# Optimization experiments

Measured on AMD Instinct MI355X. Metric: run time of the kernel, lower is better.

Reference implementation:

```python
import jax, jax.numpy as jnp
import numpy as np

N_CHROM = 23
BINS_PER_CHROM = 5000
B = 16
S = 512  # sampled bins per (class, batch-row): 256 nonzeros + 256 sampled zeros
EOS_DIM = 512
BIN_DIM = 256
D_MODEL = 512
NUM_STATES = 3
VOCAB = N_CHROM * BINS_PER_CHROM


def setup_inputs() -> dict:
    key = jax.random.key(0)
    ks = jax.random.split(key, 9)
    return {
        "eos_emb": jax.random.normal(ks[0], (B, N_CHROM, EOS_DIM), dtype=jnp.float32),
        "sampled_indices": jax.random.randint(ks[1], (N_CHROM, B, S), 0, BINS_PER_CHROM),
        "targets": jax.random.randint(ks[2], (N_CHROM, B, S), 0, 3),
        "bin_embedding_table": jax.random.normal(ks[3], (VOCAB, BIN_DIM), dtype=jnp.float32) * 0.02,
        "W_bin": jax.random.normal(ks[4], (D_MODEL, BIN_DIM), dtype=jnp.float32) / np.sqrt(BIN_DIM),
        "W_eos": jax.random.normal(ks[5], (D_MODEL, EOS_DIM), dtype=jnp.float32) / np.sqrt(EOS_DIM),
        "b_eos": jax.random.normal(ks[6], (D_MODEL,), dtype=jnp.float32) * 0.01,
        "W_fc": jax.random.normal(ks[7], (NUM_STATES, 2 * D_MODEL), dtype=jnp.float32) / np.sqrt(2 * D_MODEL),
        "b_fc": jax.random.normal(ks[8], (NUM_STATES,), dtype=jnp.float32) * 0.01,
    }


def reference(eos_emb, sampled_indices, targets, bin_embedding_table, W_bin, W_eos, b_eos, W_fc, b_fc):
    # eos_projection (use_eos_proj=True): [B, C, eos_dim] -> [B, C, d_model]
    eos = jnp.einsum("bce,de->bcd", eos_emb, W_eos) + b_eos
    # vocab index per class: token_to_ind offset c*BINS_PER_CHROM + bin position
    offsets = (jnp.arange(N_CHROM, dtype=sampled_indices.dtype) * BINS_PER_CHROM)[:, None, None]
    ind = sampled_indices + offsets                      # [C, B, S]
    bin_emb = bin_embedding_table[ind]                   # [C, B, S, bin_dim]
    # bin_projection fires because bin_emb_dim != d_model (no bias)
    bin_proj = jnp.einsum("cbse,de->cbsd", bin_emb, W_bin)  # [C, B, S, d_model]
    # repeat eos_emb[:, c, :] across each row's sampled bins
    eos_rep = jnp.broadcast_to(jnp.transpose(eos, (1, 0, 2))[:, :, None, :], bin_proj.shape)
    total = jnp.concatenate([bin_proj, eos_rep], axis=-1)   # [C, B, S, 2*d_model]
    # fc: Linear(2*d_model, num_states) + ReLU
    pred = jax.nn.relu(jnp.einsum("cbsd,nd->cbsn", total, W_fc) + b_fc)
    return pred, targets
```

## Files before the change

kernel.cpp:

```cpp
#include <hip/hip_runtime.h>

#define N_CHROM 23
#define BINS_PER_CHROM 5000
#define BSZ 16
#define SSZ 512
#define EOS_DIM 512
#define BIN_DIM 256
#define D_MODEL 512
#define VOCAB (N_CHROM * BINS_PER_CHROM)
#define ROWS (N_CHROM * BSZ * SSZ)
#define PRED_SIZE (ROWS * 3)

#define WS_M    0
#define WS_MEOS 768
#define WS_PT   3456

__global__ __launch_bounds__(256) void precompute_M(
    const float* __restrict__ W_bin, const float* __restrict__ W_eos,
    const float* __restrict__ W_fc, float* __restrict__ M,
    float* __restrict__ Meos)
{
    __shared__ float wfc_s[3][512];
    __shared__ float red[3][8][32];
    const int bid = blockIdx.x;
    const bool isM = (bid < 8);
    const float* src = isM ? W_bin : W_eos;
    const int ld   = isM ? 256 : 512;
    const int wofs = isM ? 0 : 512;
    const int eb   = (isM ? bid : (bid - 8)) * 32;
    float* dst = isM ? M : Meos;

    const int t = threadIdx.x;
    for (int i = t; i < 3 * 512; i += 256) {
        int n = i >> 9, d = i & 511;
        wfc_s[n][d] = W_fc[n * 1024 + wofs + d];
    }
    __syncthreads();

    const int el = t & 31, slice = t >> 5;
    const int e = eb + el;
    float a0 = 0.f, a1 = 0.f, a2 = 0.f;
    const int d0 = slice * 64;
    for (int dd = 0; dd < 64; ++dd) {
        int d = d0 + dd;
        float v = src[d * ld + e];
        a0 += wfc_s[0][d] * v;
        a1 += wfc_s[1][d] * v;
        a2 += wfc_s[2][d] * v;
    }
    red[0][slice][el] = a0;
    red[1][slice][el] = a1;
    red[2][slice][el] = a2;
    __syncthreads();

    if (slice < 3) {
        float s = 0.f;
        for (int q = 0; q < 8; ++q) s += red[slice][q][el];
        dst[slice * ld + e] = s;
    }
}

__global__ __launch_bounds__(256) void project_table(
    const float* __restrict__ table, const float* __restrict__ M,
    float4* __restrict__ pt)
{
    const int wave = threadIdx.x >> 6, lane = threadIdx.x & 63;
    const int rbase = (blockIdx.x * 4 + wave) * 8;
    if (rbase >= VOCAB) return;

    const float4 m0 = ((const float4*)M)[lane];
    const float4 m1 = ((const float4*)M)[64 + lane];
    const float4 m2 = ((const float4*)M)[128 + lane];

    const float4* tb = (const float4*)table;
    float4 v[8];
#pragma unroll
    for (int k = 0; k < 8; ++k)
        v[k] = tb[(long long)(rbase + k) * 64 + lane];

#pragma unroll
    for (int k = 0; k < 8; ++k) {
        float p0 = v[k].x * m0.x + v[k].y * m0.y + v[k].z * m0.z + v[k].w * m0.w;
        float p1 = v[k].x * m1.x + v[k].y * m1.y + v[k].z * m1.z + v[k].w * m1.w;
        float p2 = v[k].x * m2.x + v[k].y * m2.y + v[k].z * m2.z + v[k].w * m2.w;
        for (int m = 32; m; m >>= 1) {
            p0 += __shfl_xor(p0, m);
            p1 += __shfl_xor(p1, m);
            p2 += __shfl_xor(p2, m);
        }
        if (lane == 0) pt[rbase + k] = make_float4(p0, p1, p2, 0.f);
    }
}

__global__ __launch_bounds__(256) void gather_out(
    const int* __restrict__ sampled, const int* __restrict__ targets,
    const float4* __restrict__ pt, const float* __restrict__ Meos,
    const float* __restrict__ eos_emb, const float* __restrict__ b_eos,
    const float* __restrict__ W_fc, const float* __restrict__ b_fc,
    float* __restrict__ out)
{
    __shared__ float ebc_s[3];
    const int r = blockIdx.x * 256 + threadIdx.x;
    const int cb = blockIdx.x >> 1;
    const int c = cb / BSZ, b = cb % BSZ;

    const int bin = sampled[r];
    const int tgt = targets[r];

    const int w = threadIdx.x >> 6, lane = threadIdx.x & 63;
    if (w < 3) {
        const float* eos = eos_emb + ((long long)b * N_CHROM + c) * EOS_DIM;
        const float* me  = Meos + w * 512;
        const float* wf2 = W_fc + w * 1024 + 512;
        float s = 0.f;
#pragma unroll
        for (int e0 = 0; e0 < 512; e0 += 64) {
            int e = e0 + lane;
            s += eos[e] * me[e] + wf2[e] * b_eos[e];
        }
        for (int m = 32; m; m >>= 1) s += __shfl_xor(s, m);
        if (lane == 0) ebc_s[w] = s + b_fc[w];
    }
    __syncthreads();

    const float4 p = pt[c * BINS_PER_CHROM + bin];
    const long long o = (long long)r * 3;
    out[o + 0] = fmaxf(p.x + ebc_s[0], 0.f);
    out[o + 1] = fmaxf(p.y + ebc_s[1], 0.f);
    out[o + 2] = fmaxf(p.z + ebc_s[2], 0.f);
    out[PRED_SIZE + r] = (float)tgt;
}

extern "C" void kernel_launch(void* const* d_in, const int* in_sizes, int n_in,
                              void* d_out, int out_size, void* d_ws, size_t ws_size,
                              hipStream_t stream) {
    const float* eos_emb = (const float*)d_in[0];
    const int*   sampled = (const int*)d_in[1];
    const int*   targets = (const int*)d_in[2];
    const float* table   = (const float*)d_in[3];
    const float* W_bin   = (const float*)d_in[4];
    const float* W_eos   = (const float*)d_in[5];
    const float* b_eos   = (const float*)d_in[6];
    const float* W_fc    = (const float*)d_in[7];
    const float* b_fc    = (const float*)d_in[8];
    float* out = (float*)d_out;
    float* ws  = (float*)d_ws;

    float*  M    = ws + WS_M;
    float*  Meos = ws + WS_MEOS;
    float4* pt   = (float4*)(ws + WS_PT);

    precompute_M<<<24, 256, 0, stream>>>(W_bin, W_eos, W_fc, M, Meos);
    project_table<<<(VOCAB / 8 + 3) / 4, 256, 0, stream>>>(table, M, pt);
    gather_out<<<ROWS / 256, 256, 0, stream>>>(sampled, targets, pt, Meos,
                                               eos_emb, b_eos, W_fc, b_fc, out);
}
```

Baseline: 203.5 us.

## Precompute per-(chrom,batch) eos bias once and use nontemporal loads/stores

Moves the eos-projection dot product out of the gather kernel, where it was recomputed by every 256-row block with a block sync. It now runs once per (chromosome, batch) pair in extra blocks prepended to the table-projection kernel, and the constant bias term is computed once in the weight precompute kernel. The table stream and the gather's index reads and output writes now use nontemporal loads and stores. The gather kernel becomes a simple load-add-store with no shared memory or barrier. This adds a few hundred small blocks to the projection launch.

```diff
diff --git a/kernel.cpp b/kernel.cpp
--- a/kernel.cpp
+++ b/kernel.cpp
@@ -10,15 +10,20 @@
 #define VOCAB (N_CHROM * BINS_PER_CHROM)
 #define ROWS (N_CHROM * BSZ * SSZ)
 #define PRED_SIZE (ROWS * 3)
+#define NCB (N_CHROM * BSZ)
 
-#define WS_M    0
-#define WS_MEOS 768
-#define WS_PT   3456
+#define WS_M     0
+#define WS_MEOS  768
+#define WS_CONST 2304
+#define WS_E     2432
+#define WS_PT    4096
+
+typedef float fvec4 __attribute__((ext_vector_type(4)));
 
 __global__ __launch_bounds__(256) void precompute_M(
     const float* __restrict__ W_bin, const float* __restrict__ W_eos,
-    const float* __restrict__ W_fc, float* __restrict__ M,
-    float* __restrict__ Meos)
+    const float* __restrict__ W_fc, const float* __restrict__ b_eos,
+    const float* __restrict__ b_fc, float* __restrict__ ws)
 {
     __shared__ float wfc_s[3][512];
     __shared__ float red[3][8][32];
@@ -28,7 +33,7 @@
     const int ld   = isM ? 256 : 512;
     const int wofs = isM ? 0 : 512;
     const int eb   = (isM ? bid : (bid - 8)) * 32;
-    float* dst = isM ? M : Meos;
+    float* dst = ws + (isM ? WS_M : WS_MEOS);
 
     const int t = threadIdx.x;
     for (int i = t; i < 3 * 512; i += 256) {
@@ -58,25 +63,58 @@
         for (int q = 0; q < 8; ++q) s += red[slice][q][el];
         dst[slice * ld + e] = s;
     }
+
+    if (bid == 0) {
+        const int wv = t >> 6, ln = t & 63;
+        if (wv < 3) {
+            const float* wf2 = W_fc + wv * 1024 + 512;
+            float s = 0.f;
+#pragma unroll
+            for (int e0 = 0; e0 < 512; e0 += 64) s += wf2[e0 + ln] * b_eos[e0 + ln];
+            for (int m = 32; m; m >>= 1) s += __shfl_xor(s, m);
+            if (ln == 0) ws[WS_CONST + wv] = s + b_fc[wv];
+        }
+    }
 }
 
 __global__ __launch_bounds__(256) void project_table(
-    const float* __restrict__ table, const float* __restrict__ M,
-    float4* __restrict__ pt)
+    const float* __restrict__ table, const float* __restrict__ eos_emb,
+    float* __restrict__ ws)
 {
+    const int bid = blockIdx.x;
+    if (bid < NCB) {
+        const int c = bid >> 4, b = bid & 15;
+        const int wv = threadIdx.x >> 6, ln = threadIdx.x & 63;
+        if (wv < 3) {
+            const float* eos = eos_emb + (b * N_CHROM + c) * EOS_DIM;
+            const float* me  = ws + WS_MEOS + wv * 512;
+            float s = 0.f;
+#pragma unroll
+            for (int e0 = 0; e0 < 512; e0 += 64) {
+                int e = e0 + ln;
+                s += eos[e] * me[e];
+            }
+            for (int m = 32; m; m >>= 1) s += __shfl_xor(s, m);
+            if (ln == 0) ws[WS_E + bid * 4 + wv] = s + ws[WS_CONST + wv];
+        }
+        return;
+    }
+
     const int wave = threadIdx.x >> 6, lane = threadIdx.x & 63;
-    const int rbase = (blockIdx.x * 4 + wave) * 8;
+    const int rbase = ((bid - NCB) * 4 + wave) * 8;
     if (rbase >= VOCAB) return;
 
-    const float4 m0 = ((const float4*)M)[lane];
-    const float4 m1 = ((const float4*)M)[64 + lane];
-    const float4 m2 = ((const float4*)M)[128 + lane];
+    const fvec4* mm = (const fvec4*)(ws + WS_M);
+    const fvec4 m0 = mm[lane];
+    const fvec4 m1 = mm[64 + lane];
+    const fvec4 m2 = mm[128 + lane];
+    fvec4* pt = (fvec4*)(ws + WS_PT);
 
-    const float4* tb = (const float4*)table;
-    float4 v[8];
+    const fvec4* tb = (const fvec4*)table;
+    fvec4 v[8];
 #pragma unroll
     for (int k = 0; k < 8; ++k)
-        v[k] = tb[(long long)(rbase + k) * 64 + lane];
+        v[k] = __builtin_nontemporal_load(&tb[(rbase + k) * 64 + lane]);
 
 #pragma unroll
     for (int k = 0; k < 8; ++k) {
@@ -88,47 +126,29 @@
             p1 += __shfl_xor(p1, m);
             p2 += __shfl_xor(p2, m);
         }
-        if (lane == 0) pt[rbase + k] = make_float4(p0, p1, p2, 0.f);
+        if (lane == 0) pt[rbase + k] = (fvec4){p0, p1, p2, 0.f};
     }
 }
 
 __global__ __launch_bounds__(256) void gather_out(
     const int* __restrict__ sampled, const int* __restrict__ targets,
-    const float4* __restrict__ pt, const float* __restrict__ Meos,
-    const float* __restrict__ eos_emb, const float* __restrict__ b_eos,
-    const float* __restrict__ W_fc, const float* __restrict__ b_fc,
-    float* __restrict__ out)
+    const float* __restrict__ ws, float* __restrict__ out)
 {
-    __shared__ float ebc_s[3];
     const int r = blockIdx.x * 256 + threadIdx.x;
     const int cb = blockIdx.x >> 1;
-    const int c = cb / BSZ, b = cb % BSZ;
+    const int c = cb >> 4;
 
-    const int bin = sampled[r];
-    const int tgt = targets[r];
+    const int bin = __builtin_nontemporal_load(&sampled[r]);
+    const int tgt = __builtin_nontemporal_load(&targets[r]);
 
-    const int w = threadIdx.x >> 6, lane = threadIdx.x & 63;
-    if (w < 3) {
-        const float* eos = eos_emb + ((long long)b * N_CHROM + c) * EOS_DIM;
-        const float* me  = Meos + w * 512;
-        const float* wf2 = W_fc + w * 1024 + 512;
-        float s = 0.f;
-#pragma unroll
-        for (int e0 = 0; e0 < 512; e0 += 64) {
-            int e = e0 + lane;
-            s += eos[e] * me[e] + wf2[e] * b_eos[e];
-        }
-        for (int m = 32; m; m >>= 1) s += __shfl_xor(s, m);
-        if (lane == 0) ebc_s[w] = s + b_fc[w];
-    }
-    __syncthreads();
+    const fvec4 e = ((const fvec4*)(ws + WS_E))[cb];
+    const fvec4 p = ((const fvec4*)(ws + WS_PT))[c * BINS_PER_CHROM + bin];
 
-    const float4 p = pt[c * BINS_PER_CHROM + bin];
-    const long long o = (long long)r * 3;
-    out[o + 0] = fmaxf(p.x + ebc_s[0], 0.f);
-    out[o + 1] = fmaxf(p.y + ebc_s[1], 0.f);
-    out[o + 2] = fmaxf(p.z + ebc_s[2], 0.f);
-    out[PRED_SIZE + r] = (float)tgt;
+    const int o = r * 3;
+    __builtin_nontemporal_store(fmaxf(p.x + e.x, 0.f), &out[o + 0]);
+    __builtin_nontemporal_store(fmaxf(p.y + e.y, 0.f), &out[o + 1]);
+    __builtin_nontemporal_store(fmaxf(p.z + e.z, 0.f), &out[o + 2]);
+    __builtin_nontemporal_store((float)tgt, &out[PRED_SIZE + r]);
 }
 
 extern "C" void kernel_launch(void* const* d_in, const int* in_sizes, int n_in,
@@ -146,12 +166,7 @@
     float* out = (float*)d_out;
     float* ws  = (float*)d_ws;
 
-    float*  M    = ws + WS_M;
-    float*  Meos = ws + WS_MEOS;
-    float4* pt   = (float4*)(ws + WS_PT);
-
-    precompute_M<<<24, 256, 0, stream>>>(W_bin, W_eos, W_fc, M, Meos);
-    project_table<<<(VOCAB / 8 + 3) / 4, 256, 0, stream>>>(table, M, pt);
-    gather_out<<<ROWS / 256, 256, 0, stream>>>(sampled, targets, pt, Meos,
-                                               eos_emb, b_eos, W_fc, b_fc, out);
+    precompute_M<<<24, 256, 0, stream>>>(W_bin, W_eos, W_fc, b_eos, b_fc, ws);
+    project_table<<<NCB + (VOCAB / 8 + 3) / 4, 256, 0, stream>>>(table, eos_emb, ws);
+    gather_out<<<ROWS / 256, 256, 0, stream>>>(sampled, targets, ws, out);
 }
```

New measurement: 198.2 us. -2.6%, faster.
